# Kernel tuning notes

Hardware: AMD Instinct MI355X
Metric: run time of the kernel (lower is better)

The kernel has to match this reference:

```python
import jax, jax.numpy as jnp
import numpy as np

U, I, D, OUT = 8192, 16384, 64, 64

def setup_inputs() -> dict:
    key = jax.random.key(0)
    k1, k2, k3, k4 = jax.random.split(key, 4)
    user_emb = jax.random.normal(k1, (U, D), dtype=jnp.float32)
    item_emb = jax.random.normal(k2, (I, D), dtype=jnp.float32)
    attention_weight = jax.random.normal(k3, (D, OUT), dtype=jnp.float32) * (1.0 / np.sqrt(D))
    adj_matrix = jax.random.randint(k4, (U, I), 0, 2, dtype=jnp.int32)
    return {"user_emb": user_emb, "item_emb": item_emb,
            "attention_weight": attention_weight, "adj_matrix": adj_matrix}

def reference(user_emb, item_emb, attention_weight, adj_matrix):
    # score[u,i] = <user_emb[u], item_emb[i]>  (torch.inner)
    score = jnp.einsum('ud,id->ui', user_emb, item_emb)
    # mask non-edges to 0 (NOT -inf, faithful to torch.where(adj>0, score, 0))
    score = jnp.where(adj_matrix > 0, score, 0.0)
    score = jax.nn.softmax(score, axis=1)
    # flag == True path: aggregate items into users, then project
    output = score @ item_emb          # [U, D]
    output = output @ attention_weight  # [U, OUT]
    return output
```

## Files before the change

### kernel.cpp

```cpp
#include <hip/hip_runtime.h>
#include <hip/hip_bf16.h>
#include <math.h>

#define U_N   8192
#define I_N   16384
#define D_N   64
#define OUT_N 64
#define BN    32
#define NCH   8
#define ITERS 64
#define VN_ST 72
#define VT_ST 36
#define PL_ST 40

typedef _Float16 half8  __attribute__((ext_vector_type(8)));
typedef short    bf16x8 __attribute__((ext_vector_type(8)));
typedef short    bf16x4 __attribute__((ext_vector_type(4)));
typedef float    f32x4  __attribute__((ext_vector_type(4)));

static __device__ __forceinline__ unsigned short f2bf(float f) {
    union { __hip_bfloat16 h; unsigned short u; } cv;
    cv.h = __float2bfloat16(f);
    return cv.u;
}
static __device__ __forceinline__ float rsum16(float v) {
    #pragma unroll
    for (int o = 1; o < 16; o <<= 1) v += __shfl_xor(v, o);
    return v;
}
static __device__ __forceinline__ void bar() {
    asm volatile("s_waitcnt lgkmcnt(0)\n\ts_barrier" ::: "memory");
}

__global__ __launch_bounds__(256)
void prep_items(const float* __restrict__ item,
                _Float16* __restrict__ itemH,
                unsigned short* __restrict__ itemTt)
{
    const int i = blockIdx.x * 256 + threadIdx.x;
    const float* src = item + (size_t)i * D_N;
    f32x4 v[16];
    #pragma unroll
    for (int j = 0; j < 16; ++j) v[j] = *(const f32x4*)(src + 4 * j);

    #pragma unroll
    for (int j = 0; j < 8; ++j) {
        half8 h;
        #pragma unroll
        for (int k = 0; k < 4; ++k) { h[k] = (_Float16)v[2*j][k]; h[4+k] = (_Float16)v[2*j+1][k]; }
        *(half8*)&itemH[(size_t)i * D_N + 8 * j] = h;
    }
    const size_t tb = (size_t)(i >> 5) * (D_N * 32) + (i & 31);
    #pragma unroll
    for (int d = 0; d < 64; ++d)
        itemTt[tb + (size_t)d * 32] = f2bf(v[d >> 2][d & 3]);
}

#define DECL_SET(S) \
    int adj##S##0, adj##S##1, adj##S##2, adj##S##3, \
        adj##S##4, adj##S##5, adj##S##6, adj##S##7;  \
    half8 vn##S; bf16x8 vt##S;

#define LOAD_ADJ(S, tidx) do { \
    const size_t o_ = (size_t)(tidx) * BN; \
    adj##S##0 = adjb[0 * (size_t)I_N + o_ +  0]; \
    adj##S##1 = adjb[0 * (size_t)I_N + o_ + 16]; \
    adj##S##2 = adjb[1 * (size_t)I_N + o_ +  0]; \
    adj##S##3 = adjb[1 * (size_t)I_N + o_ + 16]; \
    adj##S##4 = adjb[2 * (size_t)I_N + o_ +  0]; \
    adj##S##5 = adjb[2 * (size_t)I_N + o_ + 16]; \
    adj##S##6 = adjb[3 * (size_t)I_N + o_ +  0]; \
    adj##S##7 = adjb[3 * (size_t)I_N + o_ + 16]; \
} while (0)

#define LOAD_TILE(S, tidx) do { \
    const size_t o_ = (size_t)(tidx) * BN; \
    vn##S = *(const half8*)&itemH[(ibase0 + o_ + (t >> 3)) * D_N + (t & 7) * 8]; \
    vt##S = *(const bf16x8*)&itemTt[((ibase0 + o_) >> 5) * (D_N * 32) \
                                    + (size_t)(t >> 2) * 32 + (t & 3) * 8]; \
} while (0)

#define COMMIT(S, bufw) do { \
    *(half8*)&Vn[bufw][(t >> 3) * VN_ST + (t & 7) * 8] = vn##S; \
    *(bf16x4*)&Vt[bufw][(t >> 2) * VT_ST + (t & 3) * 8]     = \
        __builtin_shufflevector(vt##S, vt##S, 0, 1, 2, 3); \
    *(bf16x4*)&Vt[bufw][(t >> 2) * VT_ST + (t & 3) * 8 + 4] = \
        __builtin_shufflevector(vt##S, vt##S, 4, 5, 6, 7); \
} while (0)

#define MASK_OF(S) \
    (((adj##S##0 != 0) ? 1u : 0u)       | ((adj##S##1 != 0) ? 2u : 0u) | \
     ((adj##S##2 != 0) ? 4u : 0u)       | ((adj##S##3 != 0) ? 8u : 0u) | \
     ((adj##S##4 != 0) ? 16u : 0u)      | ((adj##S##5 != 0) ? 32u : 0u) | \
     ((adj##S##6 != 0) ? 64u : 0u)      | ((adj##S##7 != 0) ? 128u : 0u))

#define COMPUTE_REST(msk, bufr) do { \
    half8 b00 = *(const half8*)&Vn[bufr][(c)      * VN_ST      + q * 8]; \
    half8 b01 = *(const half8*)&Vn[bufr][(c)      * VN_ST + 32 + q * 8]; \
    half8 b10 = *(const half8*)&Vn[bufr][(16 + c) * VN_ST      + q * 8]; \
    half8 b11 = *(const half8*)&Vn[bufr][(16 + c) * VN_ST + 32 + q * 8]; \
    f32x4 S0 = (f32x4){0.f,0.f,0.f,0.f}; \
    f32x4 S1 = (f32x4){0.f,0.f,0.f,0.f}; \
    S0 = __builtin_amdgcn_mfma_f32_16x16x32_f16(ufrag0, b00, S0, 0, 0, 0); \
    S0 = __builtin_amdgcn_mfma_f32_16x16x32_f16(ufrag1, b01, S0, 0, 0, 0); \
    S1 = __builtin_amdgcn_mfma_f32_16x16x32_f16(ufrag0, b10, S1, 0, 0, 0); \
    S1 = __builtin_amdgcn_mfma_f32_16x16x32_f16(ufrag1, b11, S1, 0, 0, 0); \
    float e_; \
    e_ = __expf(((msk) &   1u) ? S0[0] : 0.0f); S0[0] = e_; l0 += e_; \
    e_ = __expf(((msk) &   2u) ? S1[0] : 0.0f); S1[0] = e_; l0 += e_; \
    e_ = __expf(((msk) &   4u) ? S0[1] : 0.0f); S0[1] = e_; l1 += e_; \
    e_ = __expf(((msk) &   8u) ? S1[1] : 0.0f); S1[1] = e_; l1 += e_; \
    e_ = __expf(((msk) &  16u) ? S0[2] : 0.0f); S0[2] = e_; l2 += e_; \
    e_ = __expf(((msk) &  32u) ? S1[2] : 0.0f); S1[2] = e_; l2 += e_; \
    e_ = __expf(((msk) &  64u) ? S0[3] : 0.0f); S0[3] = e_; l3 += e_; \
    e_ = __expf(((msk) & 128u) ? S1[3] : 0.0f); S1[3] = e_; l3 += e_; \
    plw[(4*q+0)*PL_ST +  0 + c] = f2bf(S0[0]); \
    plw[(4*q+0)*PL_ST + 16 + c] = f2bf(S1[0]); \
    plw[(4*q+1)*PL_ST +  0 + c] = f2bf(S0[1]); \
    plw[(4*q+1)*PL_ST + 16 + c] = f2bf(S1[1]); \
    plw[(4*q+2)*PL_ST +  0 + c] = f2bf(S0[2]); \
    plw[(4*q+2)*PL_ST + 16 + c] = f2bf(S1[2]); \
    plw[(4*q+3)*PL_ST +  0 + c] = f2bf(S0[3]); \
    plw[(4*q+3)*PL_ST + 16 + c] = f2bf(S1[3]); \
    bf16x8 pf = *(const bf16x8*)&plw[c * PL_ST + q * 8]; \
    bf16x4 va0 = *(const bf16x4*)&Vt[bufr][(c)      * VT_ST + q * 8]; \
    bf16x4 vb0 = *(const bf16x4*)&Vt[bufr][(c)      * VT_ST + q * 8 + 4]; \
    bf16x4 va1 = *(const bf16x4*)&Vt[bufr][(16 + c) * VT_ST + q * 8]; \
    bf16x4 vb1 = *(const bf16x4*)&Vt[bufr][(16 + c) * VT_ST + q * 8 + 4]; \
    bf16x4 va2 = *(const bf16x4*)&Vt[bufr][(32 + c) * VT_ST + q * 8]; \
    bf16x4 vb2 = *(const bf16x4*)&Vt[bufr][(32 + c) * VT_ST + q * 8 + 4]; \
    bf16x4 va3 = *(const bf16x4*)&Vt[bufr][(48 + c) * VT_ST + q * 8]; \
    bf16x4 vb3 = *(const bf16x4*)&Vt[bufr][(48 + c) * VT_ST + q * 8 + 4]; \
    bf16x8 v0 = __builtin_shufflevector(va0, vb0, 0,1,2,3,4,5,6,7); \
    bf16x8 v1 = __builtin_shufflevector(va1, vb1, 0,1,2,3,4,5,6,7); \
    bf16x8 v2 = __builtin_shufflevector(va2, vb2, 0,1,2,3,4,5,6,7); \
    bf16x8 v3 = __builtin_shufflevector(va3, vb3, 0,1,2,3,4,5,6,7); \
    O0 = __builtin_amdgcn_mfma_f32_16x16x32_bf16(pf, v0, O0, 0, 0, 0); \
    O1 = __builtin_amdgcn_mfma_f32_16x16x32_bf16(pf, v1, O1, 0, 0, 0); \
    O2 = __builtin_amdgcn_mfma_f32_16x16x32_bf16(pf, v2, O2, 0, 0, 0); \
    O3 = __builtin_amdgcn_mfma_f32_16x16x32_bf16(pf, v3, O3, 0, 0, 0); \
} while (0)

__global__ __launch_bounds__(256, 3)
void atten_main(const float* __restrict__ user_emb,
                const _Float16* __restrict__ itemH,
                const unsigned short* __restrict__ itemTt,
                const int*   __restrict__ adj,
                float* __restrict__ wsO,
                float* __restrict__ wsL)
{
    __shared__ _Float16 Vn[2][BN * VN_ST];
    __shared__ short    Vt[2][D_N * VT_ST];
    __shared__ unsigned short Pl[4][16 * PL_ST];

    const int ch   = blockIdx.x;
    const int ub   = blockIdx.y;
    const int t    = threadIdx.x;
    const int w    = t >> 6;
    const int lane = t & 63;
    const int c    = lane & 15;
    const int q    = lane >> 4;

    const int    urow0  = ub * 64 + w * 16;
    const size_t ibase0 = (size_t)ch * (I_N / NCH);

    unsigned short* plw = &Pl[w][0];

    half8 ufrag0, ufrag1;
    {
        const float* up = user_emb + (size_t)(urow0 + c) * D_N + q * 8;
        f32x4 a0 = *(const f32x4*)(up);
        f32x4 b0 = *(const f32x4*)(up + 4);
        f32x4 a1 = *(const f32x4*)(up + 32);
        f32x4 b1 = *(const f32x4*)(up + 36);
        #pragma unroll
        for (int j = 0; j < 4; ++j) {
            ufrag0[j] = (_Float16)a0[j]; ufrag0[4 + j] = (_Float16)b0[j];
            ufrag1[j] = (_Float16)a1[j]; ufrag1[4 + j] = (_Float16)b1[j];
        }
    }

    f32x4 O0 = (f32x4){0.f,0.f,0.f,0.f};
    f32x4 O1 = O0, O2 = O0, O3 = O0;
    float l0 = 0.f, l1 = 0.f, l2 = 0.f, l3 = 0.f;

    const int* adjb = adj + (size_t)(urow0 + 4 * q) * I_N + ibase0 + c;

    DECL_SET(A)
    DECL_SET(B)

    LOAD_TILE(A, 0); LOAD_ADJ(A, 0);
    LOAD_TILE(B, 1); LOAD_ADJ(B, 1);
    COMMIT(A, 0);
    LOAD_TILE(A, 2);
    bar();

    for (int k = 0; k < ITERS; k += 2) {
        {
            const unsigned msk = MASK_OF(A);
            COMMIT(B, 1);
            const int ia = (k + 2 < ITERS) ? k + 2 : ITERS - 1;
            const int iv = (k + 3 < ITERS) ? k + 3 : ITERS - 1;
            LOAD_ADJ(A, ia);
            LOAD_TILE(B, iv);
            COMPUTE_REST(msk, 0);
            bar();
        }
        {
            const unsigned msk = MASK_OF(B);
            COMMIT(A, 0);
            const int ia = (k + 3 < ITERS) ? k + 3 : ITERS - 1;
            const int iv = (k + 4 < ITERS) ? k + 4 : ITERS - 1;
            LOAD_ADJ(B, ia);
            LOAD_TILE(A, iv);
            COMPUTE_REST(msk, 1);
            bar();
        }
    }

    l0 = rsum16(l0); l1 = rsum16(l1); l2 = rsum16(l2); l3 = rsum16(l3);

    {
        float* d0 = wsO + ((size_t)ch * U_N + urow0 + 4 * q + 0) * D_N;
        float* d1 = wsO + ((size_t)ch * U_N + urow0 + 4 * q + 1) * D_N;
        float* d2 = wsO + ((size_t)ch * U_N + urow0 + 4 * q + 2) * D_N;
        float* d3 = wsO + ((size_t)ch * U_N + urow0 + 4 * q + 3) * D_N;
        d0[c] = O0[0]; d0[16 + c] = O1[0]; d0[32 + c] = O2[0]; d0[48 + c] = O3[0];
        d1[c] = O0[1]; d1[16 + c] = O1[1]; d1[32 + c] = O2[1]; d1[48 + c] = O3[1];
        d2[c] = O0[2]; d2[16 + c] = O1[2]; d2[32 + c] = O2[2]; d2[48 + c] = O3[2];
        d3[c] = O0[3]; d3[16 + c] = O1[3]; d3[32 + c] = O2[3]; d3[48 + c] = O3[3];
    }
    if (c == 0) {
        float* lw = wsL + (size_t)ch * U_N + urow0 + 4 * q;
        lw[0] = l0; lw[1] = l1; lw[2] = l2; lw[3] = l3;
    }
}

__global__ __launch_bounds__(256)
void atten_combine(const float* __restrict__ wsO,
                   const float* __restrict__ wsL,
                   const float* __restrict__ attw,
                   float* __restrict__ out,
                   int nch)
{
    __shared__ float inv[64];
    __shared__ float agg[64][68];
    __shared__ float Wl[64][68];

    const int t  = threadIdx.x;
    const int u0 = blockIdx.x * 64;

    {
        const int d = t >> 2, o0 = (t & 3) * 16;
        const float* src = attw + d * OUT_N + o0;
        #pragma unroll
        for (int j = 0; j < 4; ++j)
            *(f32x4*)&Wl[d][o0 + 4 * j] = *(const f32x4*)(src + 4 * j);
    }
    if (t < 64) {
        float L = 0.f;
        for (int cc = 0; cc < nch; ++cc) L += wsL[(size_t)cc * U_N + u0 + t];
        inv[t] = 1.0f / L;
    }
    __syncthreads();

    {
        const int ul = t >> 2, d0 = (t & 3) * 16;
        const int u = u0 + ul;
        f32x4 a4[4];
        #pragma unroll
        for (int j = 0; j < 4; ++j) a4[j] = (f32x4){0.f, 0.f, 0.f, 0.f};
        for (int cc = 0; cc < nch; ++cc) {
            const float* src = wsO + ((size_t)cc * U_N + u) * D_N + d0;
            #pragma unroll
            for (int j = 0; j < 4; ++j) a4[j] += *(const f32x4*)(src + 4 * j);
        }
        const float s = inv[ul];
        #pragma unroll
        for (int j = 0; j < 4; ++j)
            *(f32x4*)&agg[ul][d0 + 4 * j] = a4[j] * s;
    }
    __syncthreads();

    {
        const int ul = t >> 2, o0 = (t & 3) * 16;
        f32x4 acc[4];
        #pragma unroll
        for (int j = 0; j < 4; ++j) acc[j] = (f32x4){0.f, 0.f, 0.f, 0.f};
        for (int d = 0; d < 64; ++d) {
            const float av = agg[ul][d];
            #pragma unroll
            for (int j = 0; j < 4; ++j) {
                f32x4 wv = *(const f32x4*)&Wl[d][o0 + 4 * j];
                acc[j] += wv * av;
            }
        }
        float* dst = out + (size_t)(u0 + ul) * OUT_N + o0;
        #pragma unroll
        for (int j = 0; j < 4; ++j)
            *(f32x4*)(dst + 4 * j) = acc[j];
    }
}

extern "C" void kernel_launch(void* const* d_in, const int* in_sizes, int n_in,
                              void* d_out, int out_size, void* d_ws, size_t ws_size,
                              hipStream_t stream)
{
    const float* user_emb = (const float*)d_in[0];
    const float* item_emb = (const float*)d_in[1];
    const float* attw     = (const float*)d_in[2];
    const int*   adj      = (const int*)d_in[3];
    float* out = (float*)d_out;

    float*          wsO    = (float*)d_ws;
    float*          wsL    = wsO + (size_t)NCH * U_N * D_N;
    _Float16*       itemH  = (_Float16*)(wsL + (size_t)NCH * U_N);
    unsigned short* itemTt = (unsigned short*)(itemH + (size_t)I_N * D_N);

    prep_items<<<dim3(I_N / 256), 256, 0, stream>>>(item_emb, itemH, itemTt);
    atten_main<<<dim3(NCH, U_N / 64), 256, 0, stream>>>(user_emb, itemH, itemTt, adj,
                                                        wsO, wsL);
    atten_combine<<<dim3(U_N / 64), 256, 0, stream>>>(wsO, wsL, attw, out, NCH);
}
```

Before: 723.8 us.

## Transpose score MFMA so each lane owns one user row and vectorize adj loads

Swaps the operand order of the score MFMA so each lane's accumulator holds four consecutive items for a single user row. This allows the adjacency mask to be read as two 16-byte int4 loads instead of eight scalar loads, the P tile to be written with two 8-byte stores instead of eight 2-byte stores, and the row-sum reduction to drop to two shuffles. The Vt LDS row stride is padded to 40 so the transposed value tile can be written and read as single 16-byte vectors. The cost is a different LDS bank pattern for Vt and wider per-lane adjacency registers.

```diff
diff --git a/kernel.cpp b/kernel.cpp
--- a/kernel.cpp
+++ b/kernel.cpp
@@ -10,23 +10,19 @@
 #define NCH   8
 #define ITERS 64
 #define VN_ST 72
-#define VT_ST 36
+#define VT_ST 40
 #define PL_ST 40
 
 typedef _Float16 half8  __attribute__((ext_vector_type(8)));
 typedef short    bf16x8 __attribute__((ext_vector_type(8)));
 typedef short    bf16x4 __attribute__((ext_vector_type(4)));
 typedef float    f32x4  __attribute__((ext_vector_type(4)));
+typedef int      int4v  __attribute__((ext_vector_type(4)));
 
 static __device__ __forceinline__ unsigned short f2bf(float f) {
     union { __hip_bfloat16 h; unsigned short u; } cv;
     cv.h = __float2bfloat16(f);
     return cv.u;
-}
-static __device__ __forceinline__ float rsum16(float v) {
-    #pragma unroll
-    for (int o = 1; o < 16; o <<= 1) v += __shfl_xor(v, o);
-    return v;
 }
 static __device__ __forceinline__ void bar() {
     asm volatile("s_waitcnt lgkmcnt(0)\n\ts_barrier" ::: "memory");
@@ -57,20 +53,13 @@
 }
 
 #define DECL_SET(S) \
-    int adj##S##0, adj##S##1, adj##S##2, adj##S##3, \
-        adj##S##4, adj##S##5, adj##S##6, adj##S##7;  \
+    int4v adj##S##a, adj##S##b; \
     half8 vn##S; bf16x8 vt##S;
 
 #define LOAD_ADJ(S, tidx) do { \
     const size_t o_ = (size_t)(tidx) * BN; \
-    adj##S##0 = adjb[0 * (size_t)I_N + o_ +  0]; \
-    adj##S##1 = adjb[0 * (size_t)I_N + o_ + 16]; \
-    adj##S##2 = adjb[1 * (size_t)I_N + o_ +  0]; \
-    adj##S##3 = adjb[1 * (size_t)I_N + o_ + 16]; \
-    adj##S##4 = adjb[2 * (size_t)I_N + o_ +  0]; \
-    adj##S##5 = adjb[2 * (size_t)I_N + o_ + 16]; \
-    adj##S##6 = adjb[3 * (size_t)I_N + o_ +  0]; \
-    adj##S##7 = adjb[3 * (size_t)I_N + o_ + 16]; \
+    adj##S##a = *(const int4v*)&adjq[o_];      \
+    adj##S##b = *(const int4v*)&adjq[o_ + 16]; \
 } while (0)
 
 #define LOAD_TILE(S, tidx) do { \
@@ -82,59 +71,43 @@
 
 #define COMMIT(S, bufw) do { \
     *(half8*)&Vn[bufw][(t >> 3) * VN_ST + (t & 7) * 8] = vn##S; \
-    *(bf16x4*)&Vt[bufw][(t >> 2) * VT_ST + (t & 3) * 8]     = \
-        __builtin_shufflevector(vt##S, vt##S, 0, 1, 2, 3); \
-    *(bf16x4*)&Vt[bufw][(t >> 2) * VT_ST + (t & 3) * 8 + 4] = \
-        __builtin_shufflevector(vt##S, vt##S, 4, 5, 6, 7); \
-} while (0)
-
-#define MASK_OF(S) \
-    (((adj##S##0 != 0) ? 1u : 0u)       | ((adj##S##1 != 0) ? 2u : 0u) | \
-     ((adj##S##2 != 0) ? 4u : 0u)       | ((adj##S##3 != 0) ? 8u : 0u) | \
-     ((adj##S##4 != 0) ? 16u : 0u)      | ((adj##S##5 != 0) ? 32u : 0u) | \
-     ((adj##S##6 != 0) ? 64u : 0u)      | ((adj##S##7 != 0) ? 128u : 0u))
-
-#define COMPUTE_REST(msk, bufr) do { \
-    half8 b00 = *(const half8*)&Vn[bufr][(c)      * VN_ST      + q * 8]; \
-    half8 b01 = *(const half8*)&Vn[bufr][(c)      * VN_ST + 32 + q * 8]; \
-    half8 b10 = *(const half8*)&Vn[bufr][(16 + c) * VN_ST      + q * 8]; \
-    half8 b11 = *(const half8*)&Vn[bufr][(16 + c) * VN_ST + 32 + q * 8]; \
-    f32x4 S0 = (f32x4){0.f,0.f,0.f,0.f}; \
-    f32x4 S1 = (f32x4){0.f,0.f,0.f,0.f}; \
-    S0 = __builtin_amdgcn_mfma_f32_16x16x32_f16(ufrag0, b00, S0, 0, 0, 0); \
-    S0 = __builtin_amdgcn_mfma_f32_16x16x32_f16(ufrag1, b01, S0, 0, 0, 0); \
-    S1 = __builtin_amdgcn_mfma_f32_16x16x32_f16(ufrag0, b10, S1, 0, 0, 0); \
-    S1 = __builtin_amdgcn_mfma_f32_16x16x32_f16(ufrag1, b11, S1, 0, 0, 0); \
+    *(bf16x8*)&Vt[bufw][(t >> 2) * VT_ST + (t & 3) * 8] = vt##S; \
+} while (0)
+
+#define MASKS(S, ma, mb) \
+    const unsigned ma = ((adj##S##a[0] != 0) ? 1u : 0u) | ((adj##S##a[1] != 0) ? 2u : 0u) | \
+                        ((adj##S##a[2] != 0) ? 4u : 0u) | ((adj##S##a[3] != 0) ? 8u : 0u); \
+    const unsigned mb = ((adj##S##b[0] != 0) ? 1u : 0u) | ((adj##S##b[1] != 0) ? 2u : 0u) | \
+                        ((adj##S##b[2] != 0) ? 4u : 0u) | ((adj##S##b[3] != 0) ? 8u : 0u);
+
+#define COMPUTE_REST(ma, mb, bufr) do { \
+    half8 a00 = *(const half8*)&Vn[bufr][(c)      * VN_ST      + q * 8]; \
+    half8 a01 = *(const half8*)&Vn[bufr][(c)      * VN_ST + 32 + q * 8]; \
+    half8 a10 = *(const half8*)&Vn[bufr][(16 + c) * VN_ST      + q * 8]; \
+    half8 a11 = *(const half8*)&Vn[bufr][(16 + c) * VN_ST + 32 + q * 8]; \
+    bf16x8 v0 = *(const bf16x8*)&Vt[bufr][(c)      * VT_ST + q * 8]; \
+    bf16x8 v1 = *(const bf16x8*)&Vt[bufr][(16 + c) * VT_ST + q * 8]; \
+    bf16x8 v2 = *(const bf16x8*)&Vt[bufr][(32 + c) * VT_ST + q * 8]; \
+    bf16x8 v3 = *(const bf16x8*)&Vt[bufr][(48 + c) * VT_ST + q * 8]; \
+    f32x4 T0 = (f32x4){0.f,0.f,0.f,0.f}; \
+    f32x4 T1 = (f32x4){0.f,0.f,0.f,0.f}; \
+    T0 = __builtin_amdgcn_mfma_f32_16x16x32_f16(a00, ufrag0, T0, 0, 0, 0); \
+    T0 = __builtin_amdgcn_mfma_f32_16x16x32_f16(a01, ufrag1, T0, 0, 0, 0); \
+    T1 = __builtin_amdgcn_mfma_f32_16x16x32_f16(a10, ufrag0, T1, 0, 0, 0); \
+    T1 = __builtin_amdgcn_mfma_f32_16x16x32_f16(a11, ufrag1, T1, 0, 0, 0); \
+    bf16x4 p0, p1; \
     float e_; \
-    e_ = __expf(((msk) &   1u) ? S0[0] : 0.0f); S0[0] = e_; l0 += e_; \
-    e_ = __expf(((msk) &   2u) ? S1[0] : 0.0f); S1[0] = e_; l0 += e_; \
-    e_ = __expf(((msk) &   4u) ? S0[1] : 0.0f); S0[1] = e_; l1 += e_; \
-    e_ = __expf(((msk) &   8u) ? S1[1] : 0.0f); S1[1] = e_; l1 += e_; \
-    e_ = __expf(((msk) &  16u) ? S0[2] : 0.0f); S0[2] = e_; l2 += e_; \
-    e_ = __expf(((msk) &  32u) ? S1[2] : 0.0f); S1[2] = e_; l2 += e_; \
-    e_ = __expf(((msk) &  64u) ? S0[3] : 0.0f); S0[3] = e_; l3 += e_; \
-    e_ = __expf(((msk) & 128u) ? S1[3] : 0.0f); S1[3] = e_; l3 += e_; \
-    plw[(4*q+0)*PL_ST +  0 + c] = f2bf(S0[0]); \
-    plw[(4*q+0)*PL_ST + 16 + c] = f2bf(S1[0]); \
-    plw[(4*q+1)*PL_ST +  0 + c] = f2bf(S0[1]); \
-    plw[(4*q+1)*PL_ST + 16 + c] = f2bf(S1[1]); \
-    plw[(4*q+2)*PL_ST +  0 + c] = f2bf(S0[2]); \
-    plw[(4*q+2)*PL_ST + 16 + c] = f2bf(S1[2]); \
-    plw[(4*q+3)*PL_ST +  0 + c] = f2bf(S0[3]); \
-    plw[(4*q+3)*PL_ST + 16 + c] = f2bf(S1[3]); \
+    e_ = __expf(((ma) & 1u) ? T0[0] : 0.0f); p0[0] = (short)f2bf(e_); lc += e_; \
+    e_ = __expf(((ma) & 2u) ? T0[1] : 0.0f); p0[1] = (short)f2bf(e_); lc += e_; \
+    e_ = __expf(((ma) & 4u) ? T0[2] : 0.0f); p0[2] = (short)f2bf(e_); lc += e_; \
+    e_ = __expf(((ma) & 8u) ? T0[3] : 0.0f); p0[3] = (short)f2bf(e_); lc += e_; \
+    e_ = __expf(((mb) & 1u) ? T1[0] : 0.0f); p1[0] = (short)f2bf(e_); lc += e_; \
+    e_ = __expf(((mb) & 2u) ? T1[1] : 0.0f); p1[1] = (short)f2bf(e_); lc += e_; \
+    e_ = __expf(((mb) & 4u) ? T1[2] : 0.0f); p1[2] = (short)f2bf(e_); lc += e_; \
+    e_ = __expf(((mb) & 8u) ? T1[3] : 0.0f); p1[3] = (short)f2bf(e_); lc += e_; \
+    *(bf16x4*)&plw[c * PL_ST + 4 * q]      = p0; \
+    *(bf16x4*)&plw[c * PL_ST + 16 + 4 * q] = p1; \
     bf16x8 pf = *(const bf16x8*)&plw[c * PL_ST + q * 8]; \
-    bf16x4 va0 = *(const bf16x4*)&Vt[bufr][(c)      * VT_ST + q * 8]; \
-    bf16x4 vb0 = *(const bf16x4*)&Vt[bufr][(c)      * VT_ST + q * 8 + 4]; \
-    bf16x4 va1 = *(const bf16x4*)&Vt[bufr][(16 + c) * VT_ST + q * 8]; \
-    bf16x4 vb1 = *(const bf16x4*)&Vt[bufr][(16 + c) * VT_ST + q * 8 + 4]; \
-    bf16x4 va2 = *(const bf16x4*)&Vt[bufr][(32 + c) * VT_ST + q * 8]; \
-    bf16x4 vb2 = *(const bf16x4*)&Vt[bufr][(32 + c) * VT_ST + q * 8 + 4]; \
-    bf16x4 va3 = *(const bf16x4*)&Vt[bufr][(48 + c) * VT_ST + q * 8]; \
-    bf16x4 vb3 = *(const bf16x4*)&Vt[bufr][(48 + c) * VT_ST + q * 8 + 4]; \
-    bf16x8 v0 = __builtin_shufflevector(va0, vb0, 0,1,2,3,4,5,6,7); \
-    bf16x8 v1 = __builtin_shufflevector(va1, vb1, 0,1,2,3,4,5,6,7); \
-    bf16x8 v2 = __builtin_shufflevector(va2, vb2, 0,1,2,3,4,5,6,7); \
-    bf16x8 v3 = __builtin_shufflevector(va3, vb3, 0,1,2,3,4,5,6,7); \
     O0 = __builtin_amdgcn_mfma_f32_16x16x32_bf16(pf, v0, O0, 0, 0, 0); \
     O1 = __builtin_amdgcn_mfma_f32_16x16x32_bf16(pf, v1, O1, 0, 0, 0); \
     O2 = __builtin_amdgcn_mfma_f32_16x16x32_bf16(pf, v2, O2, 0, 0, 0); \
@@ -182,9 +155,9 @@
 
     f32x4 O0 = (f32x4){0.f,0.f,0.f,0.f};
     f32x4 O1 = O0, O2 = O0, O3 = O0;
-    float l0 = 0.f, l1 = 0.f, l2 = 0.f, l3 = 0.f;
-
-    const int* adjb = adj + (size_t)(urow0 + 4 * q) * I_N + ibase0 + c;
+    float lc = 0.f;
+
+    const int* adjq = adj + (size_t)(urow0 + c) * I_N + ibase0 + 4 * q;
 
     DECL_SET(A)
     DECL_SET(B)
@@ -197,28 +170,29 @@
 
     for (int k = 0; k < ITERS; k += 2) {
         {
-            const unsigned msk = MASK_OF(A);
+            MASKS(A, ma, mb)
             COMMIT(B, 1);
             const int ia = (k + 2 < ITERS) ? k + 2 : ITERS - 1;
             const int iv = (k + 3 < ITERS) ? k + 3 : ITERS - 1;
             LOAD_ADJ(A, ia);
             LOAD_TILE(B, iv);
-            COMPUTE_REST(msk, 0);
+            COMPUTE_REST(ma, mb, 0);
             bar();
         }
         {
-            const unsigned msk = MASK_OF(B);
+            MASKS(B, ma, mb)
             COMMIT(A, 0);
             const int ia = (k + 3 < ITERS) ? k + 3 : ITERS - 1;
             const int iv = (k + 4 < ITERS) ? k + 4 : ITERS - 1;
             LOAD_ADJ(B, ia);
             LOAD_TILE(A, iv);
-            COMPUTE_REST(msk, 1);
+            COMPUTE_REST(ma, mb, 1);
             bar();
         }
     }
 
-    l0 = rsum16(l0); l1 = rsum16(l1); l2 = rsum16(l2); l3 = rsum16(l3);
+    lc += __shfl_xor(lc, 16);
+    lc += __shfl_xor(lc, 32);
 
     {
         float* d0 = wsO + ((size_t)ch * U_N + urow0 + 4 * q + 0) * D_N;
@@ -230,10 +204,8 @@
         d2[c] = O0[2]; d2[16 + c] = O1[2]; d2[32 + c] = O2[2]; d2[48 + c] = O3[2];
         d3[c] = O0[3]; d3[16 + c] = O1[3]; d3[32 + c] = O2[3]; d3[48 + c] = O3[3];
     }
-    if (c == 0) {
-        float* lw = wsL + (size_t)ch * U_N + urow0 + 4 * q;
-        lw[0] = l0; lw[1] = l1; lw[2] = l2; lw[3] = l3;
-    }
+    if (q == 0)
+        wsL[(size_t)ch * U_N + urow0 + c] = lc;
 }
 
 __global__ __launch_bounds__(256)
```

New measurement: 713.9 us. No clear change (-1.4%).
